# Performance work log

Hardware: AMD Instinct MI355X
Metric: run time of the kernel (lower is better)

The kernel has to match this reference:

```python
import jax, jax.numpy as jnp
import numpy as np

BS, SEQ, DIM, DIM_MLP, E = 2, 2048, 1024, 4096, 8
STD = 0.02  # nn.init.normal_(weight, std=0.02)


def setup_inputs() -> dict:
    key = jax.random.key(0)
    k_x, k_idx, k_w1, k_w2 = jax.random.split(key, 4)
    x = jax.random.normal(k_x, (BS, SEQ, DIM), dtype=jnp.float32)
    expert_idx = jax.random.randint(k_idx, (BS, SEQ), 0, E, dtype=jnp.int32)
    W1 = jax.random.normal(k_w1, (E, DIM, DIM_MLP), dtype=jnp.float32) * STD
    b1 = jnp.zeros((E, DIM_MLP), dtype=jnp.float32)
    W2 = jax.random.normal(k_w2, (E, DIM_MLP, DIM), dtype=jnp.float32) * STD
    b2 = jnp.zeros((E, DIM), dtype=jnp.float32)
    return {"x": x, "expert_idx": expert_idx, "W1": W1, "b1": b1, "W2": W2, "b2": b2}


def reference(x, expert_idx, W1, b1, W2, b2):
    # Compute ALL experts on all tokens (faithful to the torch module).
    # h: [bs, seq, E, dim_mlp]
    h = jnp.einsum("bsd,edm->bsem", x, W1) + b1
    h = jax.nn.gelu(h, approximate=False)  # torch nn.GELU default = exact erf
    # feat: [bs, seq, E, dim]  (== torch.cat along feature dim, reshaped)
    feat = jnp.einsum("bsem,emd->bsed", h, W2) + b2
    # Per-token gather of the assigned expert's output (top-1 select).
    idx = expert_idx.astype(jnp.int32)[:, :, None, None]  # [bs, seq, 1, 1]
    out = jnp.take_along_axis(feat, idx, axis=2)[:, :, 0, :]  # [bs, seq, dim]
    return out
```

## Files before the change

### kernel.cpp

```cpp
#include <hip/hip_runtime.h>
#include <hip/hip_bf16.h>
#include <math.h>

#define TOK   4096
#define DIM   1024
#define DMLP  4096
#define NE    8
#define BM    128
#define BN    128
#define BN2   64
#define BK    128
#define PADMAX (TOK + NE * BM)
#define NTILES (PADMAX / BM)

typedef __attribute__((ext_vector_type(8))) short  short8;
typedef __attribute__((ext_vector_type(4))) float  float4v;
typedef __attribute__((ext_vector_type(4))) unsigned short ushort4v;
typedef __attribute__((ext_vector_type(2))) unsigned long long ull2;

#define ASYNC16(gp, lp) __builtin_amdgcn_global_load_lds( \
    (const __attribute__((address_space(1))) unsigned int*)(gp), \
    (__attribute__((address_space(3))) unsigned int*)(lp), 16, 0, 0)

#define SWZ(R, C) (((C) & 8) | (((C) ^ (R)) & 7))
#define FRAG_OFF(R, C) ((((R) << 4) + SWZ(R, C)) << 3)
#define BOFF(C, n) ((((C) << 7) + (n)) << 3)

static __device__ __forceinline__ unsigned short f2bf(float f) {
  unsigned u = __float_as_uint(f);
  u += 0x7fffu + ((u >> 16) & 1u);
  return (unsigned short)(u >> 16);
}

static __device__ __forceinline__ float gelu_erf(float v) {
  const float x = fabsf(v) * 0.70710678118654752f;
  const float t = __builtin_amdgcn_rcpf(1.0f + 0.3275911f * x);
  const float poly = ((((1.061405429f * t - 1.453152027f) * t + 1.421413741f) * t
                       - 0.284496736f) * t + 0.254829592f) * t;
  const float erf_abs = 1.0f - poly * __expf(-x * x);
  return 0.5f * v * (1.0f + copysignf(erf_abs, v));
}

__global__ void group_kernel(const int* __restrict__ eidx,
                             int* __restrict__ perm,
                             int* __restrict__ tile_e) {
  __shared__ int cnt[NE], off[NE], len[NE], cur[NE];
  const int tid = threadIdx.x;
  if (tid < NE) cnt[tid] = 0;
  __syncthreads();
  for (int i = tid; i < TOK; i += 256) atomicAdd(&cnt[eidx[i]], 1);
  __syncthreads();
  if (tid == 0) {
    int o = 0;
    for (int e = 0; e < NE; e++) {
      off[e] = o;
      len[e] = ((cnt[e] + BM - 1) / BM) * BM;
      cur[e] = o;
      o += len[e];
    }
  }
  __syncthreads();
  for (int s = tid; s < PADMAX; s += 256) perm[s] = -1;
  __syncthreads();
  for (int i = tid; i < TOK; i += 256) {
    const int e = eidx[i];
    const int p = atomicAdd(&cur[e], 1);
    perm[p] = i;
  }
  __syncthreads();
  for (int t = tid; t < NTILES; t += 256) {
    const int row = t * BM;
    int te = -1;
    for (int e = 0; e < NE; e++)
      if (row >= off[e] && row < off[e] + len[e]) te = e;
    tile_e[t] = te;
  }
}

static __device__ __forceinline__
void convpack_body(const float* __restrict__ W, unsigned short* __restrict__ WT,
                   int K, int N, int kg, int nblk, int e, int tid) {
  const int n0 = nblk * 1024 + tid * 4;
  const float* Win = W + (size_t)e * K * N + (size_t)kg * 8 * N + n0;
  unsigned short* Wout = WT + (size_t)e * K * N + ((size_t)kg * N + n0) * 8;
  float4v v[8];
#pragma unroll
  for (int j = 0; j < 8; j++) v[j] = *(const float4v*)(Win + (size_t)j * N);
#pragma unroll
  for (int q = 0; q < 4; q++) {
    short8 g;
#pragma unroll
    for (int j = 0; j < 8; j++) g[j] = (short)f2bf(v[j][q]);
    *(short8*)(Wout + q * 8) = g;
  }
}

__global__ __launch_bounds__(256)
void prep1_kernel(const float* __restrict__ W1, unsigned short* __restrict__ W1T,
                  const float* __restrict__ x, const int* __restrict__ perm,
                  unsigned short* __restrict__ xg) {
  const int bid = blockIdx.x;
  const int tid = threadIdx.x;
  if (bid < 4096) {
    convpack_body(W1, W1T, DIM, DMLP, bid & 127, (bid >> 7) & 3, bid >> 9, tid);
  } else {
    const int slot = bid - 4096;
    const int t    = perm[slot];
    ushort4v o = (ushort4v){0, 0, 0, 0};
    if (t >= 0) {
      const float4v v = *(const float4v*)(x + (size_t)t * DIM + tid * 4);
#pragma unroll
      for (int q = 0; q < 4; q++) o[q] = f2bf(v[q]);
    }
    *(ushort4v*)(xg + (size_t)slot * DIM + tid * 4) = o;
  }
}

__global__ __launch_bounds__(256)
void gemm1_kernel(const unsigned short* __restrict__ xg,
                  const unsigned short* __restrict__ W1T,
                  const float* __restrict__ b1, const int* __restrict__ tile_e,
                  unsigned short* __restrict__ h,
                  const float* __restrict__ W2, unsigned short* __restrict__ W2T) {
  const int bt = blockIdx.y;
  const int te = tile_e[bt];
  const int n0 = blockIdx.x * BN;
  const int tid = threadIdx.x;

  __shared__ __align__(16) unsigned short SMEM[2 * BM * BK];

  if (te >= 0) {
    const unsigned short* Asrc = xg + (size_t)bt * BM * DIM;
    const unsigned short* Bsrc = W1T + (size_t)te * DIM * DMLP + (size_t)n0 * 8;

    const int rr = tid >> 4, q = tid & 15;
    const int cs = SWZ(rr, q);
    const unsigned short* a0 = Asrc + (size_t)rr * DIM + cs * 8;
    const int bC = tid >> 7, bn = tid & 127;
    const unsigned short* b0 = Bsrc + ((size_t)bC * DMLP + bn) * 8;

    const int wid = tid >> 6, lane = tid & 63;
    const int wm = (wid >> 1) * 64, wn = (wid & 1) * 64;
    const int l15 = lane & 15, quad = lane >> 4;

    float4v acc[4][4];
#pragma unroll
    for (int i = 0; i < 4; i++)
#pragma unroll
      for (int j = 0; j < 4; j++) acc[i][j] = (float4v){0.f, 0.f, 0.f, 0.f};

    for (int k0 = 0; k0 < DIM; k0 += BK) {
      const int kg0 = k0 >> 3;
#pragma unroll
      for (int t = 0; t < 8; t++)
        ASYNC16(a0 + (size_t)(16 * t) * DIM + k0, &SMEM[(t * 256 + tid) * 8]);
#pragma unroll
      for (int t = 0; t < 8; t++)
        ASYNC16(b0 + (size_t)(kg0 + 2 * t) * DMLP * 8,
                &SMEM[BM * BK + (t * 256 + tid) * 8]);
      __syncthreads();

#pragma unroll
      for (int hh = 0; hh < 4; hh++) {
        short8 a[4], b[4];
        const int C = hh * 4 + quad;
#pragma unroll
        for (int i = 0; i < 4; i++)
          a[i] = *(const short8*)&SMEM[FRAG_OFF(wm + i * 16 + l15, C)];
#pragma unroll
        for (int j = 0; j < 4; j++)
          b[j] = *(const short8*)&SMEM[BM * BK + BOFF(C, wn + j * 16 + l15)];
#pragma unroll
        for (int i = 0; i < 4; i++)
#pragma unroll
          for (int j = 0; j < 4; j++)
            acc[i][j] = __builtin_amdgcn_mfma_f32_16x16x32_bf16(a[i], b[j], acc[i][j], 0, 0, 0);
      }
      __syncthreads();
    }

#pragma unroll
    for (int i = 0; i < 4; i++) {
#pragma unroll
      for (int j = 0; j < 4; j++) {
        const int colL = wn + j * 16 + l15;
        const float bias = b1[te * DMLP + n0 + colL];
#pragma unroll
        for (int r = 0; r < 4; r++) {
          const int rowL = wm + i * 16 + quad * 4 + r;
          SMEM[rowL * BN + colL] = f2bf(gelu_erf(acc[i][j][r] + bias));
        }
      }
    }
    __syncthreads();
    const int gg = tid & 15;
    const int rb = tid >> 4;
#pragma unroll
    for (int p = 0; p < 8; p++) {
      const int rowL = rb + p * 16;
      const ull2 v = *(const ull2*)&SMEM[rowL * BN + gg * 8];
      *(ull2*)&h[(size_t)(bt * BM + rowL) * DMLP + n0 + gg * 8] = v;
    }
  }

  const int fb = bt * gridDim.x + blockIdx.x;
#pragma unroll
  for (int r = 0; r < 4; r++) {
    const int c = fb + 1280 * r;
    if (c < 4096) {
      convpack_body(W2, W2T, DMLP, DIM, c & 511, 0, c >> 9, tid);
    }
  }
}

__global__ __launch_bounds__(256)
void gemm2_kernel(const unsigned short* __restrict__ h,
                  const unsigned short* __restrict__ W2T,
                  const float* __restrict__ b2, const int* __restrict__ perm,
                  const int* __restrict__ tile_e, float* __restrict__ out) {
  const int bt = blockIdx.y;
  const int te = tile_e[bt];
  if (te < 0) return;
  const int n0 = blockIdx.x * BN2;
  const unsigned short* Asrc = h + (size_t)bt * BM * DMLP;
  const int tid = threadIdx.x;

  __shared__ __align__(16) unsigned short As[BM * BK];
  __shared__ __align__(16) unsigned short Bs[16 * BN2 * 8];

  const int rr = tid >> 4, q = tid & 15;
  const int cs = SWZ(rr, q);
  const unsigned short* a0 = Asrc + (size_t)rr * DMLP + cs * 8;
  const int bC = tid >> 6, bn = tid & 63;
  const unsigned short* b0 = W2T + (size_t)te * DMLP * DIM
                           + ((size_t)bC * DIM + n0 + bn) * 8;

  const int wid = tid >> 6, lane = tid & 63;
  const int wm = (wid >> 1) * 64, wn = (wid & 1) * 32;
  const int l15 = lane & 15, quad = lane >> 4;

  float4v acc[4][2];
#pragma unroll
  for (int i = 0; i < 4; i++)
#pragma unroll
    for (int j = 0; j < 2; j++) acc[i][j] = (float4v){0.f, 0.f, 0.f, 0.f};

  for (int k0 = 0; k0 < DMLP; k0 += BK) {
    const int kg0 = k0 >> 3;
#pragma unroll
    for (int t = 0; t < 8; t++)
      ASYNC16(a0 + (size_t)(16 * t) * DMLP + k0, &As[(t * 256 + tid) * 8]);
#pragma unroll
    for (int t = 0; t < 4; t++)
      ASYNC16(b0 + (size_t)(kg0 + 4 * t) * DIM * 8, &Bs[(t * 256 + tid) * 8]);
    __syncthreads();

#pragma unroll
    for (int hh = 0; hh < 4; hh++) {
      short8 a[4], b[2];
      const int C = hh * 4 + quad;
#pragma unroll
      for (int i = 0; i < 4; i++)
        a[i] = *(const short8*)&As[FRAG_OFF(wm + i * 16 + l15, C)];
#pragma unroll
      for (int j = 0; j < 2; j++)
        b[j] = *(const short8*)&Bs[(((C) << 6) + wn + j * 16 + l15) << 3];
#pragma unroll
      for (int i = 0; i < 4; i++)
#pragma unroll
        for (int j = 0; j < 2; j++)
          acc[i][j] = __builtin_amdgcn_mfma_f32_16x16x32_bf16(a[i], b[j], acc[i][j], 0, 0, 0);
    }
    __syncthreads();
  }

#pragma unroll
  for (int i = 0; i < 4; i++) {
#pragma unroll
    for (int j = 0; j < 2; j++) {
      const int col = n0 + wn + j * 16 + l15;
      const float bias = b2[te * DIM + col];
#pragma unroll
      for (int r = 0; r < 4; r++) {
        const int row  = wm + i * 16 + quad * 4 + r;
        const int slot = bt * BM + row;
        const int t    = perm[slot];
        if (t >= 0) out[(size_t)t * DIM + col] = acc[i][j][r] + bias;
      }
    }
  }
}

extern "C" void kernel_launch(void* const* d_in, const int* in_sizes, int n_in,
                              void* d_out, int out_size, void* d_ws, size_t ws_size,
                              hipStream_t stream) {
  const float* x    = (const float*)d_in[0];
  const int*   eidx = (const int*)d_in[1];
  const float* W1   = (const float*)d_in[2];
  const float* b1   = (const float*)d_in[3];
  const float* W2   = (const float*)d_in[4];
  const float* b2   = (const float*)d_in[5];
  float* out = (float*)d_out;

  char* ws = (char*)d_ws;
  int* perm   = (int*)ws;
  int* tile_e = (int*)(ws + PADMAX * sizeof(int));
  unsigned short* xg  = (unsigned short*)(ws + 32768);
  unsigned short* h   = (unsigned short*)(ws + 32768 + 10485760);
  unsigned short* W1T = (unsigned short*)(ws + 32768 + 10485760 + 41943040);
  unsigned short* W2T = (unsigned short*)((char*)W1T + 67108864);

  group_kernel<<<1, 256, 0, stream>>>(eidx, perm, tile_e);
  prep1_kernel<<<4096 + PADMAX, 256, 0, stream>>>(W1, W1T, x, perm, xg);
  gemm1_kernel<<<dim3(DMLP / BN, NTILES), 256, 0, stream>>>(xg, W1T, b1, tile_e, h, W2, W2T);
  gemm2_kernel<<<dim3(DIM / BN2, NTILES), 256, 0, stream>>>(h, W2T, b2, perm, tile_e, out);
}
```

Baseline: 454.4 us.

## Fold grouping into prep kernel and gather token rows inside GEMM1

Removes the separate single-block grouping launch by running it as block 0 of the prep kernel. The prep kernel now converts x to bf16 in original token order, and GEMM1 gathers A rows through perm with per-row async loads, so the permuted padded copy of x is no longer needed. The GEMM1 epilogue staging buffer in shared memory gets a padded row stride to reduce bank conflicts. Padding rows now load token 0's data instead of zeros, and those rows are computed but presumably discarded in GEMM2.

```diff
diff --git a/kernel.cpp b/kernel.cpp
--- a/kernel.cpp
+++ b/kernel.cpp
@@ -12,6 +12,7 @@
 #define BK    128
 #define PADMAX (TOK + NE * BM)
 #define NTILES (PADMAX / BM)
+#define EPAD  136
 
 typedef __attribute__((ext_vector_type(8))) short  short8;
 typedef __attribute__((ext_vector_type(4))) float  float4v;
@@ -41,11 +42,10 @@
   return 0.5f * v * (1.0f + copysignf(erf_abs, v));
 }
 
-__global__ void group_kernel(const int* __restrict__ eidx,
-                             int* __restrict__ perm,
-                             int* __restrict__ tile_e) {
+static __device__ __forceinline__
+void group_body(const int* __restrict__ eidx, int* __restrict__ perm,
+                int* __restrict__ tile_e, int tid) {
   __shared__ int cnt[NE], off[NE], len[NE], cur[NE];
-  const int tid = threadIdx.x;
   if (tid < NE) cnt[tid] = 0;
   __syncthreads();
   for (int i = tid; i < TOK; i += 256) atomicAdd(&cnt[eidx[i]], 1);
@@ -96,30 +96,32 @@
 }
 
 __global__ __launch_bounds__(256)
-void prep1_kernel(const float* __restrict__ W1, unsigned short* __restrict__ W1T,
-                  const float* __restrict__ x, const int* __restrict__ perm,
-                  unsigned short* __restrict__ xg) {
+void prep_kernel(const int* __restrict__ eidx, int* __restrict__ perm,
+                 int* __restrict__ tile_e,
+                 const float* __restrict__ W1, unsigned short* __restrict__ W1T,
+                 const float* __restrict__ x, unsigned short* __restrict__ xbf) {
   const int bid = blockIdx.x;
   const int tid = threadIdx.x;
-  if (bid < 4096) {
-    convpack_body(W1, W1T, DIM, DMLP, bid & 127, (bid >> 7) & 3, bid >> 9, tid);
+  if (bid == 0) {
+    group_body(eidx, perm, tile_e, tid);
+  } else if (bid < 4097) {
+    const int b = bid - 1;
+    convpack_body(W1, W1T, DIM, DMLP, b & 127, (b >> 7) & 3, b >> 9, tid);
   } else {
-    const int slot = bid - 4096;
-    const int t    = perm[slot];
-    ushort4v o = (ushort4v){0, 0, 0, 0};
-    if (t >= 0) {
-      const float4v v = *(const float4v*)(x + (size_t)t * DIM + tid * 4);
-#pragma unroll
-      for (int q = 0; q < 4; q++) o[q] = f2bf(v[q]);
-    }
-    *(ushort4v*)(xg + (size_t)slot * DIM + tid * 4) = o;
+    const int row = bid - 4097;
+    const float4v v = *(const float4v*)(x + (size_t)row * DIM + tid * 4);
+    ushort4v o;
+#pragma unroll
+    for (int q = 0; q < 4; q++) o[q] = f2bf(v[q]);
+    *(ushort4v*)(xbf + (size_t)row * DIM + tid * 4) = o;
   }
 }
 
 __global__ __launch_bounds__(256)
-void gemm1_kernel(const unsigned short* __restrict__ xg,
+void gemm1_kernel(const unsigned short* __restrict__ xbf,
                   const unsigned short* __restrict__ W1T,
-                  const float* __restrict__ b1, const int* __restrict__ tile_e,
+                  const float* __restrict__ b1, const int* __restrict__ perm,
+                  const int* __restrict__ tile_e,
                   unsigned short* __restrict__ h,
                   const float* __restrict__ W2, unsigned short* __restrict__ W2T) {
   const int bt = blockIdx.y;
@@ -130,12 +132,16 @@
   __shared__ __align__(16) unsigned short SMEM[2 * BM * BK];
 
   if (te >= 0) {
-    const unsigned short* Asrc = xg + (size_t)bt * BM * DIM;
     const unsigned short* Bsrc = W1T + (size_t)te * DIM * DMLP + (size_t)n0 * 8;
 
     const int rr = tid >> 4, q = tid & 15;
     const int cs = SWZ(rr, q);
-    const unsigned short* a0 = Asrc + (size_t)rr * DIM + cs * 8;
+    const unsigned short* aP[8];
+#pragma unroll
+    for (int t = 0; t < 8; t++) {
+      const int tok = perm[bt * BM + 16 * t + rr];
+      aP[t] = xbf + (size_t)(tok < 0 ? 0 : tok) * DIM + cs * 8;
+    }
     const int bC = tid >> 7, bn = tid & 127;
     const unsigned short* b0 = Bsrc + ((size_t)bC * DMLP + bn) * 8;
 
@@ -153,7 +159,7 @@
       const int kg0 = k0 >> 3;
 #pragma unroll
       for (int t = 0; t < 8; t++)
-        ASYNC16(a0 + (size_t)(16 * t) * DIM + k0, &SMEM[(t * 256 + tid) * 8]);
+        ASYNC16(aP[t] + k0, &SMEM[(t * 256 + tid) * 8]);
 #pragma unroll
       for (int t = 0; t < 8; t++)
         ASYNC16(b0 + (size_t)(kg0 + 2 * t) * DMLP * 8,
@@ -188,7 +194,7 @@
 #pragma unroll
         for (int r = 0; r < 4; r++) {
           const int rowL = wm + i * 16 + quad * 4 + r;
-          SMEM[rowL * BN + colL] = f2bf(gelu_erf(acc[i][j][r] + bias));
+          SMEM[rowL * EPAD + colL] = f2bf(gelu_erf(acc[i][j][r] + bias));
         }
       }
     }
@@ -198,7 +204,7 @@
 #pragma unroll
     for (int p = 0; p < 8; p++) {
       const int rowL = rb + p * 16;
-      const ull2 v = *(const ull2*)&SMEM[rowL * BN + gg * 8];
+      const ull2 v = *(const ull2*)&SMEM[rowL * EPAD + gg * 8];
       *(ull2*)&h[(size_t)(bt * BM + rowL) * DMLP + n0 + gg * 8] = v;
     }
   }
@@ -305,13 +311,12 @@
   char* ws = (char*)d_ws;
   int* perm   = (int*)ws;
   int* tile_e = (int*)(ws + PADMAX * sizeof(int));
-  unsigned short* xg  = (unsigned short*)(ws + 32768);
+  unsigned short* xbf = (unsigned short*)(ws + 32768);
   unsigned short* h   = (unsigned short*)(ws + 32768 + 10485760);
   unsigned short* W1T = (unsigned short*)(ws + 32768 + 10485760 + 41943040);
   unsigned short* W2T = (unsigned short*)((char*)W1T + 67108864);
 
-  group_kernel<<<1, 256, 0, stream>>>(eidx, perm, tile_e);
-  prep1_kernel<<<4096 + PADMAX, 256, 0, stream>>>(W1, W1T, x, perm, xg);
-  gemm1_kernel<<<dim3(DMLP / BN, NTILES), 256, 0, stream>>>(xg, W1T, b1, tile_e, h, W2, W2T);
+  prep_kernel<<<8193, 256, 0, stream>>>(eidx, perm, tile_e, W1, W1T, x, xbf);
+  gemm1_kernel<<<dim3(DMLP / BN, NTILES), 256, 0, stream>>>(xbf, W1T, b1, perm, tile_e, h, W2, W2T);
   gemm2_kernel<<<dim3(DIM / BN2, NTILES), 256, 0, stream>>>(h, W2T, b2, perm, tile_e, out);
 }
```

After: 445.5 us, median of 2. -2.0%, faster.
